# Optimization experiments

Measured on AMD Instinct MI355X. Metric: run time of the kernel, lower is better.

The kernel has to match this reference:

```python
import jax, jax.numpy as jnp
import numpy as np
import math

B, S, D = 4, 2048, 1024
H = 16
DH = D // H
NEG = -1e20


def setup_inputs() -> dict:
    key = jax.random.key(0)
    ks = jax.random.split(key, 8)
    Q_batch = jax.random.normal(ks[0], (B, S, D), dtype=jnp.float32)
    K_batch = jax.random.normal(ks[1], (B, S, D), dtype=jnp.float32)
    V_batch = jax.random.normal(ks[2], (B, S, D), dtype=jnp.float32)
    valid_lens = jax.random.randint(ks[3], (B,), 0, S).astype(jnp.int64)
    # LazyLinear weights, stored as (in, out) so projection is x @ W
    sc = 1.0 / math.sqrt(D)
    Wq = jax.random.normal(ks[4], (D, D), dtype=jnp.float32) * sc
    Wk = jax.random.normal(ks[5], (D, D), dtype=jnp.float32) * sc
    Wv = jax.random.normal(ks[6], (D, D), dtype=jnp.float32) * sc
    Wo = jax.random.normal(ks[7], (D, D), dtype=jnp.float32) * sc
    return {"Q_batch": Q_batch, "K_batch": K_batch, "V_batch": V_batch,
            "valid_lens": valid_lens, "Wq": Wq, "Wk": Wk, "Wv": Wv, "Wo": Wo}


def reference(Q_batch, K_batch, V_batch, valid_lens, Wq, Wk, Wv, Wo):
    b, nq, _ = Q_batch.shape
    nk = K_batch.shape[1]
    # project and split heads (feature dim split head-major, matching transpose_qkv)
    q = (Q_batch @ Wq).reshape(b, nq, H, DH).transpose(0, 2, 1, 3)  # (b,h,nq,dh)
    k = (K_batch @ Wk).reshape(b, nk, H, DH).transpose(0, 2, 1, 3)  # (b,h,nk,dh)
    v = (V_batch @ Wv).reshape(b, nk, H, DH).transpose(0, 2, 1, 3)  # (b,h,nk,dh)
    scores = jnp.einsum('bhqd,bhkd->bhqk', q, k) / math.sqrt(DH)
    # mask keys at position >= valid_lens[b] (shared across heads and queries)
    key_pos = jnp.arange(nk)
    mask = key_pos[None, None, None, :] < valid_lens[:, None, None, None]
    scores = jnp.where(mask, scores, NEG)
    w = jax.nn.softmax(scores, axis=-1)  # dropout rate 0 -> identity
    o = jnp.einsum('bhqk,bhkd->bhqd', w, v)           # (b,h,nq,dh)
    o = o.transpose(0, 2, 1, 3).reshape(b, nq, H * DH)  # concat heads
    return o @ Wo
```

## Files before the change

kernel.cpp:

```cpp
#include <hip/hip_runtime.h>
#include <stdint.h>

typedef unsigned short u16;
using bf16x8 = __attribute__((ext_vector_type(8))) __bf16;
using f32x4  = __attribute__((ext_vector_type(4))) float;
using u16x8  = __attribute__((ext_vector_type(8))) unsigned short;
using u16x4  = __attribute__((ext_vector_type(4))) unsigned short;

#define NH   16
#define DHD  64
#define SEQ  2048
#define DD   1024

__device__ inline u16 bfbits(float f) {
    __bf16 h = (__bf16)f;
    return __builtin_bit_cast(u16, h);
}

__device__ inline void gld16(const u16* g, u16* l) {
    __builtin_amdgcn_global_load_lds(
        (const __attribute__((address_space(1))) void*)g,
        (__attribute__((address_space(3))) void*)l,
        16, 0, 0);
}

__global__ __launch_bounds__(256) void transpose4(
    const float* __restrict__ s0, const float* __restrict__ s1,
    const float* __restrict__ s2, const float* __restrict__ s3,
    u16* __restrict__ d0, u16* __restrict__ d1,
    u16* __restrict__ d2, u16* __restrict__ d3)
{
    const float* src = s0; u16* dst = d0;
    if (blockIdx.z == 1) { src = s1; dst = d1; }
    else if (blockIdx.z == 2) { src = s2; dst = d2; }
    else if (blockIdx.z == 3) { src = s3; dst = d3; }

    __shared__ u16 tile[32][33];
    int tx = threadIdx.x, ty = threadIdx.y;
    int x = blockIdx.x * 32 + tx;
    int y0 = blockIdx.y * 32 + ty;
#pragma unroll
    for (int i = 0; i < 32; i += 8)
        tile[ty + i][tx] = bfbits(src[(size_t)(y0 + i) * DD + x]);
    __syncthreads();
    int x2 = blockIdx.y * 32 + tx;
    int y2 = blockIdx.x * 32 + ty;
#pragma unroll
    for (int i = 0; i < 32; i += 8)
        dst[(size_t)(y2 + i) * DD + x2] = tile[tx][ty + i];
}

__global__ __launch_bounds__(256) void cvt3(
    const float* __restrict__ s0, const float* __restrict__ s1,
    const float* __restrict__ s2,
    u16* __restrict__ d0, u16* __restrict__ d1, u16* __restrict__ d2)
{
    const float* src = s0; u16* dst = d0;
    if (blockIdx.z == 1) { src = s1; dst = d1; }
    else if (blockIdx.z == 2) { src = s2; dst = d2; }
    size_t i = ((size_t)blockIdx.x * 256 + threadIdx.x) * 8;
    f32x4 a = *(const f32x4*)&src[i];
    f32x4 b = *(const f32x4*)&src[i + 4];
    u16x8 o;
#pragma unroll
    for (int j = 0; j < 4; ++j) { o[j] = bfbits(a[j]); o[j + 4] = bfbits(b[j]); }
    *(u16x8*)&dst[i] = o;
}

__global__ __launch_bounds__(256) void cvt1(
    const float* __restrict__ src, u16* __restrict__ dst)
{
    size_t i = ((size_t)blockIdx.x * 256 + threadIdx.x) * 8;
    f32x4 a = *(const f32x4*)&src[i];
    f32x4 b = *(const f32x4*)&src[i + 4];
    u16x8 o;
#pragma unroll
    for (int j = 0; j < 4; ++j) { o[j] = bfbits(a[j]); o[j + 4] = bfbits(b[j]); }
    *(u16x8*)&dst[i] = o;
}

template<int MODE>
__global__ __launch_bounds__(256) void gemm_bt16(
    const u16* __restrict__ A0, const u16* __restrict__ A1, const u16* __restrict__ A2,
    const u16* __restrict__ B0, const u16* __restrict__ B1, const u16* __restrict__ B2,
    void* __restrict__ C0, void* __restrict__ C1, void* __restrict__ C2)
{
    const int K = 1024;
    const u16* A = A0; const u16* Bt = B0; void* C = C0;
    if (MODE == 3) {
        if (blockIdx.z == 1) { A = A1; Bt = B1; C = C1; }
        else if (blockIdx.z == 2) { A = A2; Bt = B2; C = C2; }
    }

    __shared__ __align__(16) u16 As[2][128 * 32];
    __shared__ __align__(16) u16 Bs[2][128 * 32];

    const int t = threadIdx.x;
    const int wave = t >> 6, lane = t & 63;
    const int l15 = lane & 15, q4 = lane >> 4;
    const int wm = (wave >> 1) * 64, wn = (wave & 1) * 64;

    const int gx = gridDim.x;
    const int nwg = gx * gridDim.y;
    int flat = blockIdx.y * gx + blockIdx.x;
    flat = (flat & 7) * (nwg >> 3) + (flat >> 3);
    const int m0 = (flat / gx) * 128, n0 = (flat % gx) * 128;

    const int ar = t >> 2;
    const int ac = (t & 3) * 8;

    const u16* gA = &A [(size_t)(m0 + ar) * K + ac];
    const u16* gB = &Bt[(size_t)(n0 + ar) * K + ac];
    u16* lA0 = &As[0][t * 8];
    u16* lA1 = &As[1][t * 8];
    u16* lB0 = &Bs[0][t * 8];
    u16* lB1 = &Bs[1][t * 8];

    f32x4 acc[4][4] = {};

    for (int k0 = 0; k0 < K; k0 += 64) {
        __syncthreads();
        gld16(gA + k0,                   lA0);
        gld16(gA + (size_t)64 * K + k0,  lA0 + 64 * 32);
        gld16(gA + k0 + 32,              lA1);
        gld16(gA + (size_t)64 * K + k0 + 32, lA1 + 64 * 32);
        gld16(gB + k0,                   lB0);
        gld16(gB + (size_t)64 * K + k0,  lB0 + 64 * 32);
        gld16(gB + k0 + 32,              lB1);
        gld16(gB + (size_t)64 * K + k0 + 32, lB1 + 64 * 32);
        __syncthreads();

#pragma unroll
        for (int hf = 0; hf < 2; ++hf) {
            bf16x8 af[4], bfr[4];
#pragma unroll
            for (int i = 0; i < 4; ++i) {
                af[i]  = *(const bf16x8*)&As[hf][(wm + i * 16 + l15) * 32 + q4 * 8];
                bfr[i] = *(const bf16x8*)&Bs[hf][(wn + i * 16 + l15) * 32 + q4 * 8];
            }
#pragma unroll
            for (int i = 0; i < 4; ++i)
#pragma unroll
                for (int j = 0; j < 4; ++j)
                    acc[i][j] = __builtin_amdgcn_mfma_f32_16x16x32_bf16(af[i], bfr[j], acc[i][j], 0, 0, 0);
        }
    }

    const bool vt_store = (MODE == 2) || (MODE == 3 && blockIdx.z == 2);

#pragma unroll
    for (int i = 0; i < 4; ++i) {
        int row_l = wm + i * 16 + q4 * 4;
#pragma unroll
        for (int j = 0; j < 4; ++j) {
            int col = n0 + wn + j * 16 + l15;
            if (MODE == 1) {
#pragma unroll
                for (int r = 0; r < 4; ++r) {
                    int row = m0 + row_l + r;
                    ((float*)C)[(size_t)row * DD + col] = acc[i][j][r];
                }
            } else if (vt_store) {
                int row = m0 + row_l;
                int b = row >> 11, s = row & (SEQ - 1);
                int h = col >> 6, dh = col & (DHD - 1);
                u16x4 pk;
#pragma unroll
                for (int r = 0; r < 4; ++r) pk[r] = bfbits(acc[i][j][r]);
                *(u16x4*)&((u16*)C)[(((size_t)(b * NH + h) * DHD + dh) << 11) | s] = pk;
            } else {
#pragma unroll
                for (int r = 0; r < 4; ++r) {
                    int row = m0 + row_l + r;
                    int b = row >> 11, s = row & (SEQ - 1);
                    int h = col >> 6, dh = col & (DHD - 1);
                    ((u16*)C)[(((size_t)(b * NH + h) * SEQ + s) << 6) | dh] = bfbits(acc[i][j][r]);
                }
            }
        }
    }
}

__global__ __launch_bounds__(256, 3) void attn(
    const u16* __restrict__ q_ws, const u16* __restrict__ k_ws,
    const u16* __restrict__ vT_ws, const int* __restrict__ valid_lens,
    u16* __restrict__ o_ws)
{
    const int bh = blockIdx.y;
    const int b = bh >> 4, h = bh & 15;
    const int qt = blockIdx.x;
    const int valid = valid_lens[b];
    const bool valid0 = (valid == 0);
    const int valid_eff = valid0 ? SEQ : valid;
    const int kt_n = (valid_eff + 63) >> 6;
    const float c2 = valid0 ? 0.f : 0.18033688011112042f;
    const float M2 = 17.312340490667562f;

    __shared__ __align__(16) u16 KV[2][2][64 * 64];
    __shared__ u16 Ps[4][32][72];

    const int t = threadIdx.x;
    const int wave = t >> 6, lane = t & 63;
    const int l15 = lane & 15, q4 = lane >> 4;

    const size_t base  = (size_t)bh * SEQ * DHD;
    const size_t vbase = (size_t)bh * DHD * SEQ;

    const int q0 = qt * 128 + wave * 32;

    const int sr0 = wave * 16 + (lane >> 3);
    const int cg  = ((lane & 7) ^ (sr0 & 7)) * 8;
    const u16* gK = &k_ws [base  + (size_t)sr0 * DHD + cg];
    const u16* gV = &vT_ws[vbase + (size_t)sr0 * SEQ + cg];
    const int ldst = sr0 * 64 + (lane & 7) * 8;

    u16x8 ou;
#pragma unroll
    for (int j = 0; j < 8; ++j) ou[j] = 0x3F80;
    const bf16x8 ones = __builtin_bit_cast(bf16x8, ou);

    bf16x8 qf[2][2];
#pragma unroll
    for (int mi = 0; mi < 2; ++mi)
#pragma unroll
        for (int c = 0; c < 2; ++c)
            qf[mi][c] = *(const bf16x8*)&q_ws[base + (size_t)(q0 + mi * 16 + l15) * DHD + c * 32 + q4 * 8];

    f32x4 o4[2][4] = {};
    f32x4 l_acc[2] = {};

    const int swz = (l15 & 7) * 8;

    {
        gld16(gK,                 &KV[0][0][ldst]);
        gld16(gK + 512,           &KV[0][0][ldst + 512]);
        gld16(gV,                 &KV[0][1][ldst]);
        gld16(gV + (size_t)8 * SEQ, &KV[0][1][ldst + 512]);
    }

    int cur = 0;
    for (int kt = 0; kt < kt_n; ++kt) {
        __syncthreads();
        if (kt + 1 < kt_n) {
            const u16* kk = gK + (size_t)(kt + 1) * 64 * DHD;
            const u16* vv = gV + (size_t)(kt + 1) * 64;
            int bf = cur ^ 1;
            gld16(kk,                 &KV[bf][0][ldst]);
            gld16(kk + 512,           &KV[bf][0][ldst + 512]);
            gld16(vv,                 &KV[bf][1][ldst]);
            gld16(vv + (size_t)8 * SEQ, &KV[bf][1][ldst + 512]);
        }

        const u16* KK = KV[cur][0];
        const u16* VV = KV[cur][1];

        f32x4 s4[2][4] = {};
#pragma unroll
        for (int c = 0; c < 2; ++c)
#pragma unroll
            for (int ni = 0; ni < 4; ++ni) {
                bf16x8 kf = *(const bf16x8*)&KK[(ni * 16 + l15) * 64 + ((c * 32 + q4 * 8) ^ swz)];
#pragma unroll
                for (int mi = 0; mi < 2; ++mi)
                    s4[mi][ni] = __builtin_amdgcn_mfma_f32_16x16x32_bf16(kf, qf[mi][c], s4[mi][ni], 0, 0, 0);
            }

        const bool tile_full = valid0 || (kt * 64 + 64 <= valid_eff);
        if (tile_full) {
#pragma unroll
            for (int mi = 0; mi < 2; ++mi) {
                int qrow = mi * 16 + l15;
#pragma unroll
                for (int ni = 0; ni < 4; ++ni) {
                    u16x4 pk;
#pragma unroll
                    for (int r = 0; r < 4; ++r) {
                        float p = exp2f(__builtin_fmaf(s4[mi][ni][r], c2, -M2));
                        pk[r] = bfbits(p);
                    }
                    *(u16x4*)&Ps[wave][qrow][ni * 16 + q4 * 4] = pk;
                }
            }
        } else {
#pragma unroll
            for (int mi = 0; mi < 2; ++mi) {
                int qrow = mi * 16 + l15;
#pragma unroll
                for (int ni = 0; ni < 4; ++ni) {
                    u16x4 pk;
#pragma unroll
                    for (int r = 0; r < 4; ++r) {
                        bool ok = (kt * 64 + ni * 16 + q4 * 4 + r) < valid_eff;
                        float arg = ok ? __builtin_fmaf(s4[mi][ni][r], c2, -M2) : -1e30f;
                        pk[r] = bfbits(exp2f(arg));
                    }
                    *(u16x4*)&Ps[wave][qrow][ni * 16 + q4 * 4] = pk;
                }
            }
        }

#pragma unroll
        for (int c = 0; c < 2; ++c) {
            bf16x8 pf[2];
#pragma unroll
            for (int mi = 0; mi < 2; ++mi) {
                pf[mi] = *(const bf16x8*)&Ps[wave][mi * 16 + l15][c * 32 + q4 * 8];
                l_acc[mi] = __builtin_amdgcn_mfma_f32_16x16x32_bf16(pf[mi], ones, l_acc[mi], 0, 0, 0);
            }
#pragma unroll
            for (int dt = 0; dt < 4; ++dt) {
                bf16x8 vf = *(const bf16x8*)&VV[(dt * 16 + l15) * 64 + ((c * 32 + q4 * 8) ^ swz)];
#pragma unroll
                for (int mi = 0; mi < 2; ++mi)
                    o4[mi][dt] = __builtin_amdgcn_mfma_f32_16x16x32_bf16(pf[mi], vf, o4[mi][dt], 0, 0, 0);
            }
        }
        cur ^= 1;
    }

#pragma unroll
    for (int mi = 0; mi < 2; ++mi) {
        float inv[4];
#pragma unroll
        for (int r = 0; r < 4; ++r) inv[r] = 1.0f / l_acc[mi][r];
        int qrow = q0 + mi * 16 + q4 * 4;
#pragma unroll
        for (int dt = 0; dt < 4; ++dt) {
            int dh = dt * 16 + l15;
#pragma unroll
            for (int r = 0; r < 4; ++r) {
                float v = o4[mi][dt][r] * inv[r];
                o_ws[((size_t)(b * SEQ + qrow + r) << 10) | (h * DHD + dh)] = bfbits(v);
            }
        }
    }
}

extern "C" void kernel_launch(void* const* d_in, const int* in_sizes, int n_in,
                              void* d_out, int out_size, void* d_ws, size_t ws_size,
                              hipStream_t stream)
{
    (void)in_sizes; (void)n_in; (void)out_size;
    const float* Q  = (const float*)d_in[0];
    const float* Kb = (const float*)d_in[1];
    const float* V  = (const float*)d_in[2];
    const int*   vl = (const int*)d_in[3];
    const float* Wq = (const float*)d_in[4];
    const float* Wk = (const float*)d_in[5];
    const float* Wv = (const float*)d_in[6];
    const float* Wo = (const float*)d_in[7];
    float* out = (float*)d_out;

    char* ws = (char*)d_ws;
    u16* WqT   = (u16*)(ws + (size_t)0);
    u16* WkT   = (u16*)(ws + ((size_t)2 << 20));
    u16* WvT   = (u16*)(ws + ((size_t)4 << 20));
    u16* WoT   = (u16*)(ws + ((size_t)6 << 20));
    u16* q_ws  = (u16*)(ws + ((size_t)8 << 20));
    u16* k_ws  = (u16*)(ws + ((size_t)24 << 20));
    u16* vT_ws = (u16*)(ws + ((size_t)40 << 20));
    u16* o_ws  = (u16*)(ws + ((size_t)56 << 20));
    u16* Qbf   = (u16*)(ws + ((size_t)72 << 20));
    u16* Kbf   = (u16*)(ws + ((size_t)88 << 20));
    u16* Vbf   = (u16*)(ws + ((size_t)104 << 20));

    transpose4<<<dim3(32, 32, 4), dim3(32, 8), 0, stream>>>(
        Wq, Wk, Wv, Wo, WqT, WkT, WvT, WoT);

    const bool fused = ws_size >= ((size_t)120 << 20);
    if (fused) {
        cvt3<<<dim3(4096, 1, 3), 256, 0, stream>>>(Q, Kb, V, Qbf, Kbf, Vbf);
        gemm_bt16<3><<<dim3(8, 64, 3), 256, 0, stream>>>(
            Qbf, Kbf, Vbf, WqT, WkT, WvT, q_ws, k_ws, vT_ws);
    } else {
        cvt1<<<4096, 256, 0, stream>>>(Q, o_ws);
        gemm_bt16<0><<<dim3(8, 64), 256, 0, stream>>>(
            o_ws, nullptr, nullptr, WqT, nullptr, nullptr, q_ws, nullptr, nullptr);
        cvt1<<<4096, 256, 0, stream>>>(Kb, o_ws);
        gemm_bt16<0><<<dim3(8, 64), 256, 0, stream>>>(
            o_ws, nullptr, nullptr, WkT, nullptr, nullptr, k_ws, nullptr, nullptr);
        cvt1<<<4096, 256, 0, stream>>>(V, o_ws);
        gemm_bt16<2><<<dim3(8, 64), 256, 0, stream>>>(
            o_ws, nullptr, nullptr, WvT, nullptr, nullptr, vT_ws, nullptr, nullptr);
    }

    attn<<<dim3(16, 64), 256, 0, stream>>>(q_ws, k_ws, vT_ws, vl, o_ws);

    gemm_bt16<1><<<dim3(8, 64), 256, 0, stream>>>(
        o_ws, nullptr, nullptr, WoT, nullptr, nullptr, out, nullptr, nullptr);
}
```

Baseline: 313.5 us.

## Single-buffer V tile and swizzle P scratch to fit four blocks per CU

V drops from double buffering to a single buffer that is loaded at the start of each iteration and waited on with a manual vmcnt plus barrier before the PV MFMAs. K stays double-buffered. The P scratch loses its padding and uses an XOR swizzle instead, the launch bound rises to four blocks per CU, and exp2f is replaced with the hardware exp2 intrinsic. The goal is less LDS per block and higher occupancy, but the V load latency is now exposed inside each iteration. The hand-written waitcnt and barrier also depend on the order in which loads are issued.

```diff
diff --git a/kernel.cpp b/kernel.cpp
--- a/kernel.cpp
+++ b/kernel.cpp
@@ -181,7 +181,7 @@
     }
 }
 
-__global__ __launch_bounds__(256, 3) void attn(
+__global__ __launch_bounds__(256, 4) void attn(
     const u16* __restrict__ q_ws, const u16* __restrict__ k_ws,
     const u16* __restrict__ vT_ws, const int* __restrict__ valid_lens,
     u16* __restrict__ o_ws)
@@ -196,8 +196,9 @@
     const float c2 = valid0 ? 0.f : 0.18033688011112042f;
     const float M2 = 17.312340490667562f;
 
-    __shared__ __align__(16) u16 KV[2][2][64 * 64];
-    __shared__ u16 Ps[4][32][72];
+    __shared__ __align__(16) u16 Kbuf[2][64 * 64];
+    __shared__ __align__(16) u16 Vbuf[64 * 64];
+    __shared__ __align__(16) u16 Ps[4][32][64];
 
     const int t = threadIdx.x;
     const int wave = t >> 6, lane = t & 63;
@@ -229,30 +230,28 @@
     f32x4 o4[2][4] = {};
     f32x4 l_acc[2] = {};
 
-    const int swz = (l15 & 7) * 8;
-
-    {
-        gld16(gK,                 &KV[0][0][ldst]);
-        gld16(gK + 512,           &KV[0][0][ldst + 512]);
-        gld16(gV,                 &KV[0][1][ldst]);
-        gld16(gV + (size_t)8 * SEQ, &KV[0][1][ldst + 512]);
-    }
+    const int swz  = (l15 & 7) * 8;
+
+    gld16(gK,       &Kbuf[0][ldst]);
+    gld16(gK + 512, &Kbuf[0][ldst + 512]);
 
     int cur = 0;
     for (int kt = 0; kt < kt_n; ++kt) {
         __syncthreads();
-        if (kt + 1 < kt_n) {
+        {
+            const u16* vv = gV + (size_t)kt * 64;
+            gld16(vv,                   &Vbuf[ldst]);
+            gld16(vv + (size_t)8 * SEQ, &Vbuf[ldst + 512]);
+        }
+        const bool pre = (kt + 1 < kt_n);
+        if (pre) {
             const u16* kk = gK + (size_t)(kt + 1) * 64 * DHD;
-            const u16* vv = gV + (size_t)(kt + 1) * 64;
             int bf = cur ^ 1;
-            gld16(kk,                 &KV[bf][0][ldst]);
-            gld16(kk + 512,           &KV[bf][0][ldst + 512]);
-            gld16(vv,                 &KV[bf][1][ldst]);
-            gld16(vv + (size_t)8 * SEQ, &KV[bf][1][ldst + 512]);
-        }
-
-        const u16* KK = KV[cur][0];
-        const u16* VV = KV[cur][1];
+            gld16(kk,       &Kbuf[bf][ldst]);
+            gld16(kk + 512, &Kbuf[bf][ldst + 512]);
+        }
+
+        const u16* KK = Kbuf[cur];
 
         f32x4 s4[2][4] = {};
 #pragma unroll
@@ -270,21 +269,23 @@
 #pragma unroll
             for (int mi = 0; mi < 2; ++mi) {
                 int qrow = mi * 16 + l15;
+                int psw  = (l15 & 7) * 8;
 #pragma unroll
                 for (int ni = 0; ni < 4; ++ni) {
                     u16x4 pk;
 #pragma unroll
                     for (int r = 0; r < 4; ++r) {
-                        float p = exp2f(__builtin_fmaf(s4[mi][ni][r], c2, -M2));
+                        float p = __builtin_amdgcn_exp2f(__builtin_fmaf(s4[mi][ni][r], c2, -M2));
                         pk[r] = bfbits(p);
                     }
-                    *(u16x4*)&Ps[wave][qrow][ni * 16 + q4 * 4] = pk;
+                    *(u16x4*)&Ps[wave][qrow][(ni * 16 + q4 * 4) ^ psw] = pk;
                 }
             }
         } else {
 #pragma unroll
             for (int mi = 0; mi < 2; ++mi) {
                 int qrow = mi * 16 + l15;
+                int psw  = (l15 & 7) * 8;
 #pragma unroll
                 for (int ni = 0; ni < 4; ++ni) {
                     u16x4 pk;
@@ -292,24 +293,27 @@
                     for (int r = 0; r < 4; ++r) {
                         bool ok = (kt * 64 + ni * 16 + q4 * 4 + r) < valid_eff;
                         float arg = ok ? __builtin_fmaf(s4[mi][ni][r], c2, -M2) : -1e30f;
-                        pk[r] = bfbits(exp2f(arg));
+                        pk[r] = bfbits(__builtin_amdgcn_exp2f(arg));
                     }
-                    *(u16x4*)&Ps[wave][qrow][ni * 16 + q4 * 4] = pk;
+                    *(u16x4*)&Ps[wave][qrow][(ni * 16 + q4 * 4) ^ psw] = pk;
                 }
             }
         }
+
+        if (pre) asm volatile("s_waitcnt vmcnt(2)\n\ts_barrier" ::: "memory");
+        else     asm volatile("s_waitcnt vmcnt(0)\n\ts_barrier" ::: "memory");
 
 #pragma unroll
         for (int c = 0; c < 2; ++c) {
             bf16x8 pf[2];
 #pragma unroll
             for (int mi = 0; mi < 2; ++mi) {
-                pf[mi] = *(const bf16x8*)&Ps[wave][mi * 16 + l15][c * 32 + q4 * 8];
+                pf[mi] = *(const bf16x8*)&Ps[wave][mi * 16 + l15][(c * 32 + q4 * 8) ^ ((l15 & 7) * 8)];
                 l_acc[mi] = __builtin_amdgcn_mfma_f32_16x16x32_bf16(pf[mi], ones, l_acc[mi], 0, 0, 0);
             }
 #pragma unroll
             for (int dt = 0; dt < 4; ++dt) {
-                bf16x8 vf = *(const bf16x8*)&VV[(dt * 16 + l15) * 64 + ((c * 32 + q4 * 8) ^ swz)];
+                bf16x8 vf = *(const bf16x8*)&Vbuf[(dt * 16 + l15) * 64 + ((c * 32 + q4 * 8) ^ swz)];
 #pragma unroll
                 for (int mi = 0; mi < 2; ++mi)
                     o4[mi][dt] = __builtin_amdgcn_mfma_f32_16x16x32_bf16(pf[mi], vf, o4[mi][dt], 0, 0, 0);
```

Result: faster. 303.2 us (-3.3%).
